# Performance work log

Hardware: AMD Instinct MI355X
Metric: run time of the kernel (lower is better)

The kernel has to match this reference:

```python
import jax, jax.numpy as jnp
import numpy as np

N_NODES = 50000
N_EDGES = 800000
IN_DIM = 128
HID = 32
HEADS = 4
OUT_DIM = 128
NEG_SLOPE = 0.2


def setup_inputs() -> dict:
    key = jax.random.key(0)
    ks = jax.random.split(key, 10)
    s = lambda fan_in: 1.0 / np.sqrt(fan_in)
    return {
        "x": jax.random.normal(ks[0], (N_NODES, IN_DIM), dtype=jnp.float32),
        "edge_index": jax.random.randint(ks[1], (2, N_EDGES), 0, N_NODES, dtype=jnp.int64),
        # encoder GATConv: in=IN_DIM, out=HID, heads=HEADS (concat)
        "W1": jax.random.normal(ks[2], (IN_DIM, HEADS * HID), dtype=jnp.float32) * s(IN_DIM),
        "att_src1": jax.random.normal(ks[3], (HEADS, HID), dtype=jnp.float32) * s(HID),
        "att_dst1": jax.random.normal(ks[4], (HEADS, HID), dtype=jnp.float32) * s(HID),
        "b1": jnp.zeros((HEADS * HID,), dtype=jnp.float32),
        # decoder GATConv: in=HEADS*HID, out=OUT_DIM, heads=1
        "W2": jax.random.normal(ks[5], (HEADS * HID, OUT_DIM), dtype=jnp.float32) * s(HEADS * HID),
        "att_src2": jax.random.normal(ks[6], (1, OUT_DIM), dtype=jnp.float32) * s(OUT_DIM),
        "att_dst2": jax.random.normal(ks[7], (1, OUT_DIM), dtype=jnp.float32) * s(OUT_DIM),
        "b2": jnp.zeros((OUT_DIM,), dtype=jnp.float32),
    }


def _gat_conv(x, src, dst, W, att_src, att_dst, bias, heads, out_ch):
    """PyG-style GATConv (v1), eval mode (dropout off), self-loops already in src/dst."""
    n = x.shape[0]
    h = (x @ W).reshape(n, heads, out_ch)                 # [N,H,C]
    a_src = jnp.einsum("nhc,hc->nh", h, att_src)          # [N,H]
    a_dst = jnp.einsum("nhc,hc->nh", h, att_dst)          # [N,H]
    e = jax.nn.leaky_relu(a_src[src] + a_dst[dst], NEG_SLOPE)  # [E,H]
    # segment softmax over destination neighborhoods
    e_max = jax.ops.segment_max(e, dst, num_segments=n)   # [N,H]
    e_exp = jnp.exp(e - e_max[dst])
    denom = jax.ops.segment_sum(e_exp, dst, num_segments=n)
    alpha = e_exp / (denom[dst] + 1e-16)                  # [E,H]
    msg = h[src] * alpha[:, :, None]                      # [E,H,C]
    out = jax.ops.segment_sum(msg, dst, num_segments=n)   # [N,H,C]
    return out.reshape(n, heads * out_ch) + bias


def reference(x, edge_index, W1, att_src1, att_dst1, b1, W2, att_src2, att_dst2, b2):
    n = x.shape[0]
    loops = jnp.arange(n, dtype=edge_index.dtype)
    src = jnp.concatenate([edge_index[0], loops])
    dst = jnp.concatenate([edge_index[1], loops])
    z = jax.nn.relu(_gat_conv(x, src, dst, W1, att_src1, att_dst1, b1, HEADS, HID))
    x_hat = jax.nn.relu(_gat_conv(z, src, dst, W2, att_src2, att_dst2, b2, 1, OUT_DIM))
    return x_hat
```

## Files before the change

kernel.cpp:

```cpp
#include <hip/hip_runtime.h>
#include <hip/hip_bf16.h>
#include <cstddef>

#define N_NODES 50000
#define N_EDGES_RAW 800000
#define E_TOT (N_EDGES_RAW + N_NODES)
#define DIM 128
#define NEG_SLOPE 0.2f

#define NBUCK 196
#define CHUNK 4096
#define NBLK_E ((E_TOT + CHUNK - 1) / CHUNK)
#define CONV_BLKS 3125
#define GB 782

typedef __attribute__((ext_vector_type(8))) short bf16x8;
typedef __attribute__((ext_vector_type(4))) float f32x4;

__device__ __forceinline__ ushort f2bf(float f) {
  unsigned u = __float_as_uint(f);
  return (ushort)((u + 0x7FFFu + ((u >> 16) & 1u)) >> 16);
}
__device__ __forceinline__ float bf2f_lo(uint u) {
  return __uint_as_float(u << 16);
}
__device__ __forceinline__ float bf2f_hi(uint u) {
  return __uint_as_float(u & 0xFFFF0000u);
}

__device__ __forceinline__ void get_edge(const int* __restrict__ ei, int is64,
                                         int e, int& s, int& d) {
  if (e >= N_EDGES_RAW) { s = e - N_EDGES_RAW; d = s; return; }
  if (is64) {
    s = ei[2 * (size_t)e];
    d = ei[2 * ((size_t)N_EDGES_RAW + (size_t)e)];
  } else {
    s = ei[e];
    d = ei[N_EDGES_RAW + e];
  }
}

__device__ __forceinline__ int detect_inline(const int* __restrict__ ei,
                                             int* sflag) {
  const int t = threadIdx.x;
  if (t < 64) {
    int hi = ei[2 * t + 1];
    unsigned long long b = __ballot(hi != 0);
    if (t == 0) *sflag = (b == 0ULL) ? 1 : 0;
  }
  __syncthreads();
  return *sflag;
}

__device__ __forceinline__ void prep_one(const float* __restrict__ w,
                                         const float* __restrict__ atts,
                                         const float* __restrict__ attd,
                                         ushort* __restrict__ wtx,
                                         int H, int idx) {
  const int c = idx >> 7, k = idx & 127;
  const int C = 128 / H;
  float v;
  if (c < 128) {
    v = w[k * 128 + c];
  } else if (c < 128 + H) {
    const int hd = c - 128;
    float s = 0.f;
    for (int j = 0; j < C; ++j) s += w[k * 128 + hd * C + j] * atts[hd * C + j];
    v = s;
  } else if (c < 128 + 2 * H) {
    const int hd = c - 128 - H;
    float s = 0.f;
    for (int j = 0; j < C; ++j) s += w[k * 128 + hd * C + j] * attd[hd * C + j];
    v = s;
  } else {
    v = 0.f;
  }
  wtx[idx] = f2bf(v);
}

__global__ __launch_bounds__(256) void mega_setup(
    const float* __restrict__ W1, const float* __restrict__ as1,
    const float* __restrict__ ad1, ushort* __restrict__ wtx1,
    const float* __restrict__ W2, const float* __restrict__ as2,
    const float* __restrict__ ad2, ushort* __restrict__ wtx2,
    const float* __restrict__ x, ushort* __restrict__ x_bf,
    const int* __restrict__ ei, int* __restrict__ hist_mat,
    unsigned* __restrict__ pairs) {
  const int b = blockIdx.x, t = threadIdx.x;
  if (b < 72) {
    prep_one(W1, as1, ad1, wtx1, 4, b * 256 + t);
  } else if (b < 144) {
    prep_one(W2, as2, ad2, wtx2, 1, (b - 72) * 256 + t);
  } else if (b < 144 + CONV_BLKS) {
    const int base = (b - 144) * 2048 + t * 8;
    float4 v0 = *(const float4*)(x + base);
    float4 v1 = *(const float4*)(x + base + 4);
    ushort u[8];
    u[0] = f2bf(v0.x); u[1] = f2bf(v0.y); u[2] = f2bf(v0.z); u[3] = f2bf(v0.w);
    u[4] = f2bf(v1.x); u[5] = f2bf(v1.y); u[6] = f2bf(v1.z); u[7] = f2bf(v1.w);
    *(uint4*)(x_bf + base) = *(const uint4*)u;
  } else {
    __shared__ int hist[NBUCK];
    __shared__ int sflag;
    const int cb = b - 144 - CONV_BLKS;
    if (t < NBUCK) hist[t] = 0;
    const int is64 = detect_inline(ei, &sflag);
    __syncthreads();
    const int e0 = cb * CHUNK;
#pragma unroll
    for (int i = 0; i < CHUNK / 256; ++i) {
      int e = e0 + i * 256 + t;
      if (e < E_TOT) {
        int s, d;
        get_edge(ei, is64, e, s, d);
        pairs[e] = (unsigned)s | ((unsigned)d << 16);
        atomicAdd(&hist[d >> 8], 1);
      }
    }
    __syncthreads();
    if (t < NBUCK) hist_mat[cb * NBUCK + t] = hist[t];
  }
}

__global__ __launch_bounds__(256) void bucket_scatter(
    const unsigned* __restrict__ pairs, const int* __restrict__ hist_mat,
    unsigned* __restrict__ tmp, int* __restrict__ bstart_g) {
  __shared__ int wtot[4];
  __shared__ int sbase[NBUCK];
  __shared__ int shist[NBUCK];
  const int b = blockIdx.x, t = threadIdx.x, lane = t & 63, wid = t >> 6;
  int tot = 0, pre = 0;
  if (t < NBUCK) {
    for (int bb = 0; bb < NBLK_E; ++bb) {
      int v = hist_mat[bb * NBUCK + t];
      pre += (bb < b) ? v : 0;
      tot += v;
    }
    shist[t] = 0;
  }
  int sc = tot;
#pragma unroll
  for (int m = 1; m < 64; m <<= 1) {
    int o = __shfl_up(sc, m, 64);
    if (lane >= m) sc += o;
  }
  if (lane == 63) wtot[wid] = sc;
  __syncthreads();
  int off = 0;
  for (int w = 0; w < wid; ++w) off += wtot[w];
  const int excl = off + sc - tot;
  if (t < NBUCK) sbase[t] = excl + pre;
  if (b == 0) {
    if (t < NBUCK) bstart_g[t] = excl;
    if (t == 255) bstart_g[NBUCK] = off + sc;
  }
  __syncthreads();
  const int e0 = b * CHUNK;
  unsigned pr_[CHUNK / 256];
  int rk[CHUNK / 256];
#pragma unroll
  for (int i = 0; i < CHUNK / 256; ++i) {
    int e = e0 + i * 256 + t;
    if (e < E_TOT) {
      unsigned pr = pairs[e];
      pr_[i] = pr;
      rk[i] = atomicAdd(&shist[pr >> 24], 1);
    }
  }
#pragma unroll
  for (int i = 0; i < CHUNK / 256; ++i) {
    int e = e0 + i * 256 + t;
    if (e < E_TOT) tmp[sbase[pr_[i] >> 24] + rk[i]] = pr_[i];
  }
}

__device__ __forceinline__ void bucket_sort_body(int b,
                                                 const unsigned* __restrict__ tmp,
                                                 const int* __restrict__ bstart,
                                                 unsigned* __restrict__ csr2,
                                                 int* __restrict__ rp,
                                                 int* __restrict__ deg) {
  __shared__ int cnt[256];
  __shared__ int cur[256];
  __shared__ int wtot2[4];
  const int t = threadIdx.x, lane = t & 63, wid = t >> 6;
  const int p0 = bstart[b], p1 = bstart[b + 1];
  cnt[t] = 0;
  __syncthreads();
  for (int j = p0 + t; j < p1; j += 256) {
    unsigned pr = tmp[j];
    atomicAdd(&cnt[(pr >> 16) & 255u], 1);
  }
  __syncthreads();
  int v = cnt[t];
  int sc = v;
#pragma unroll
  for (int m = 1; m < 64; m <<= 1) {
    int o = __shfl_up(sc, m, 64);
    if (lane >= m) sc += o;
  }
  if (lane == 63) wtot2[wid] = sc;
  __syncthreads();
  int off = 0;
  for (int w = 0; w < wid; ++w) off += wtot2[w];
  const int excl = off + sc - v;
  const int node = b * 256 + t;
  if (node < N_NODES) {
    deg[node] = v;
    rp[node] = p0 + excl;
  }
  cur[t] = excl;
  __syncthreads();
  for (int j = p0 + t; j < p1; j += 256) {
    unsigned pr = tmp[j];
    int ld = (int)((pr >> 16) & 255u);
    int r = atomicAdd(&cur[ld], 1);
    csr2[p0 + r] = pr;
  }
}

template <int H>
__device__ __forceinline__ void gemm_att_body(int blk,
                                              const ushort* __restrict__ in_bf,
                                              const ushort* __restrict__ wtx,
                                              ushort* __restrict__ h_bf,
                                              float* __restrict__ a_src,
                                              float* __restrict__ a_dst) {
  const int wid = threadIdx.x >> 6;
  const int lane = threadIdx.x & 63;
  const int tile = blk * 4 + wid;
  if (tile >= N_NODES / 16) return;
  const int row0 = tile * 16;
  const int rA = lane & 15;
  const int g = lane >> 4;

  f32x4 acc[9];
#pragma unroll
  for (int ct = 0; ct < 9; ++ct) acc[ct] = (f32x4){0.f, 0.f, 0.f, 0.f};

#pragma unroll
  for (int ks = 0; ks < 4; ++ks) {
    const int k0 = ks * 32 + g * 8;
    bf16x8 af = *(const bf16x8*)(in_bf + (size_t)(row0 + rA) * DIM + k0);
#pragma unroll
    for (int ct = 0; ct < 9; ++ct) {
      bf16x8 bf = *(const bf16x8*)(wtx + (size_t)(ct * 16 + rA) * 128 + k0);
      acc[ct] = __builtin_amdgcn_mfma_f32_16x16x32_bf16(af, bf, acc[ct], 0, 0, 0);
    }
  }

#pragma unroll
  for (int ct = 0; ct < 8; ++ct) {
#pragma unroll
    for (int r = 0; r < 4; ++r) {
      const int row = row0 + g * 4 + r;
      h_bf[(size_t)row * DIM + ct * 16 + rA] = f2bf(acc[ct][r]);
    }
  }
  if (rA < 2 * H) {
#pragma unroll
    for (int r = 0; r < 4; ++r) {
      const int row = row0 + g * 4 + r;
      if (rA < H)
        a_src[(size_t)row * H + rA] = acc[8][r];
      else
        a_dst[(size_t)row * H + (rA - H)] = acc[8][r];
    }
  }
}

__global__ __launch_bounds__(256) void gemm4_sort(
    const ushort* __restrict__ x_bf, const ushort* __restrict__ wtx1,
    ushort* __restrict__ h_bf, float* __restrict__ a_src,
    float* __restrict__ a_dst, const unsigned* __restrict__ tmp,
    const int* __restrict__ bstart, unsigned* __restrict__ csr2,
    int* __restrict__ rp, int* __restrict__ deg) {
  if (blockIdx.x < GB)
    gemm_att_body<4>(blockIdx.x, x_bf, wtx1, h_bf, a_src, a_dst);
  else
    bucket_sort_body(blockIdx.x - GB, tmp, bstart, csr2, rp, deg);
}

__global__ __launch_bounds__(256) void gemm_att1(const ushort* __restrict__ in_bf,
                                                 const ushort* __restrict__ wtx,
                                                 ushort* __restrict__ h_bf,
                                                 float* __restrict__ a_src,
                                                 float* __restrict__ a_dst) {
  gemm_att_body<1>(blockIdx.x, in_bf, wtx, h_bf, a_src, a_dst);
}

template <int H, bool OBF>
__global__ __launch_bounds__(256) void node_agg(const int* __restrict__ rp,
                                                const int* __restrict__ deg,
                                                const unsigned* __restrict__ csr2,
                                                const ushort* __restrict__ h_bf,
                                                const float* __restrict__ a_src,
                                                const float* __restrict__ a_dst,
                                                const float* __restrict__ bias,
                                                void* __restrict__ outp) {
  __shared__ float p_lds[4][H][68];
  __shared__ int s_lds[4][64];
  const int wid = threadIdx.x >> 6;
  const int lane = threadIdx.x & 63;
  const int node = blockIdx.x * 4 + wid;
  if (node >= N_NODES) return;
  const int head = (H == 4) ? (lane >> 4) : 0;
  const int beg = rp[node];
  const int dg = deg[node];

  float ad[H];
#pragma unroll
  for (int h = 0; h < H; ++h) ad[h] = a_dst[(size_t)node * H + h];

  float sden = 0.f, ax = 0.f, ay = 0.f;

  for (int c0 = 0; c0 < dg; c0 += 64) {
    const int cnt = min(64, dg - c0);
    if (lane < cnt) {
      int s = (int)(csr2[beg + c0 + lane] & 0xFFFFu);
      s_lds[wid][lane] = s;
      if (H == 4) {
        float4 as4 = ((const float4*)a_src)[s];
        float vv[4] = {as4.x, as4.y, as4.z, as4.w};
#pragma unroll
        for (int h = 0; h < 4; ++h) {
          float v = vv[h] + ad[h];
          v = v > 0.f ? v : NEG_SLOPE * v;
          v = fminf(fmaxf(v, -60.f), 80.f);
          p_lds[wid][h][lane] = __expf(v);
        }
      } else {
        float v = a_src[s] + ad[0];
        v = v > 0.f ? v : NEG_SLOPE * v;
        v = fminf(fmaxf(v, -60.f), 80.f);
        p_lds[wid][0][lane] = __expf(v);
      }
    }
    int j = 0;
    for (; j + 8 <= cnt; j += 8) {
#pragma unroll
      for (int u = 0; u < 8; ++u) {
        int s = s_lds[wid][j + u];
        float p = p_lds[wid][head][j + u];
        uint hv = *(const uint*)(h_bf + (size_t)s * DIM + 2 * lane);
        ax += p * bf2f_lo(hv);
        ay += p * bf2f_hi(hv);
        sden += p;
      }
    }
    for (; j < cnt; ++j) {
      int s = s_lds[wid][j];
      float p = p_lds[wid][head][j];
      uint hv = *(const uint*)(h_bf + (size_t)s * DIM + 2 * lane);
      ax += p * bf2f_lo(hv);
      ay += p * bf2f_hi(hv);
      sden += p;
    }
  }

  const float inv = 1.f / sden;
  float2 bv = ((const float2*)bias)[lane];
  float ox = fmaxf(ax * inv + bv.x, 0.f);
  float oy = fmaxf(ay * inv + bv.y, 0.f);
  if (OBF) {
    uint u = (uint)f2bf(ox) | ((uint)f2bf(oy) << 16);
    ((uint*)((ushort*)outp + (size_t)node * DIM))[lane] = u;
  } else {
    ((float2*)((float*)outp + (size_t)node * DIM))[lane] = make_float2(ox, oy);
  }
}

extern "C" void kernel_launch(void* const* d_in, const int* in_sizes, int n_in,
                              void* d_out, int out_size, void* d_ws, size_t ws_size,
                              hipStream_t stream) {
  const float* x   = (const float*)d_in[0];
  const int*   ei  = (const int*)d_in[1];
  const float* W1  = (const float*)d_in[2];
  const float* as1 = (const float*)d_in[3];
  const float* ad1 = (const float*)d_in[4];
  const float* b1  = (const float*)d_in[5];
  const float* W2  = (const float*)d_in[6];
  const float* as2 = (const float*)d_in[7];
  const float* ad2 = (const float*)d_in[8];
  const float* b2  = (const float*)d_in[9];
  float* out = (float*)d_out;

  char* ws = (char*)d_ws;
  const size_t F_H = (size_t)N_NODES * DIM;
  ushort*   h_bf    = (ushort*)ws;
  ushort*   z_bf    = h_bf + F_H;
  ushort*   x_bf    = z_bf + F_H;
  float*    a_src   = (float*)(x_bf + F_H);
  float*    a_dst   = a_src + 200000;
  int*      deg     = (int*)(a_dst + 200000);
  int*      rp      = deg + N_NODES;
  unsigned* csr2    = (unsigned*)(rp + N_NODES);
  unsigned* tmp     = csr2 + E_TOT;
  unsigned* pairs   = tmp + E_TOT;
  int*      hist_mat= (int*)(pairs + E_TOT);
  int*      bstart  = hist_mat + NBLK_E * NBUCK;
  ushort*   wtx1    = (ushort*)(bstart + NBUCK + 3);
  ushort*   wtx2    = wtx1 + 144 * 128;

  const int MEGA = 144 + CONV_BLKS + NBLK_E;
  const int AGG_B = (N_NODES + 3) / 4;

  hipLaunchKernelGGL(mega_setup, dim3(MEGA), dim3(256), 0, stream,
                     W1, as1, ad1, wtx1, W2, as2, ad2, wtx2, x, x_bf, ei,
                     hist_mat, pairs);
  hipLaunchKernelGGL(bucket_scatter, dim3(NBLK_E), dim3(256), 0, stream,
                     pairs, hist_mat, tmp, bstart);
  hipLaunchKernelGGL(gemm4_sort, dim3(GB + NBUCK), dim3(256), 0, stream,
                     x_bf, wtx1, h_bf, a_src, a_dst, tmp, bstart, csr2, rp, deg);
  hipLaunchKernelGGL((node_agg<4, true>), dim3(AGG_B), dim3(256), 0, stream,
                     rp, deg, csr2, h_bf, a_src, a_dst, b1, z_bf);

  hipLaunchKernelGGL(gemm_att1, dim3(GB), dim3(256), 0, stream,
                     z_bf, wtx2, h_bf, a_src, a_dst);
  hipLaunchKernelGGL((node_agg<1, false>), dim3(AGG_B), dim3(256), 0, stream,
                     rp, deg, csr2, h_bf, a_src, a_dst, b2, out);
}
```

Baseline: 164.1 us.

## Reorder decoder layer to aggregate first, then apply W2 in the aggregation epilogue

```diff
diff --git a/kernel.cpp b/kernel.cpp
--- a/kernel.cpp
+++ b/kernel.cpp
@@ -79,20 +79,35 @@
 }
 
 __global__ __launch_bounds__(256) void mega_setup(
+    const int* __restrict__ ei, int* __restrict__ hist_mat,
+    unsigned* __restrict__ pairs,
     const float* __restrict__ W1, const float* __restrict__ as1,
-    const float* __restrict__ ad1, ushort* __restrict__ wtx1,
+    const float* __restrict__ ad1,
     const float* __restrict__ W2, const float* __restrict__ as2,
-    const float* __restrict__ ad2, ushort* __restrict__ wtx2,
+    const float* __restrict__ ad2,
     const float* __restrict__ x, ushort* __restrict__ x_bf,
-    const int* __restrict__ ei, int* __restrict__ hist_mat,
-    unsigned* __restrict__ pairs) {
+    ushort* __restrict__ wtx1, ushort* __restrict__ wtx2,
+    float* __restrict__ w_as2, float* __restrict__ w_ad2) {
   const int b = blockIdx.x, t = threadIdx.x;
   if (b < 72) {
     prep_one(W1, as1, ad1, wtx1, 4, b * 256 + t);
-  } else if (b < 144) {
-    prep_one(W2, as2, ad2, wtx2, 1, (b - 72) * 256 + t);
-  } else if (b < 144 + CONV_BLKS) {
-    const int base = (b - 144) * 2048 + t * 8;
+  } else if (b < 136) {
+    const int idx = (b - 72) * 256 + t;
+    const int c = idx >> 7, k = idx & 127;
+    wtx2[idx] = f2bf(W2[k * 128 + c]);
+  } else if (b == 136) {
+    if (t < 128) {
+      float s2 = 0.f, d2 = 0.f;
+      for (int c = 0; c < 128; ++c) {
+        float w = W2[t * 128 + c];
+        s2 += w * as2[c];
+        d2 += w * ad2[c];
+      }
+      w_as2[t] = s2;
+      w_ad2[t] = d2;
+    }
+  } else if (b < 137 + CONV_BLKS) {
+    const int base = (b - 137) * 2048 + t * 8;
     float4 v0 = *(const float4*)(x + base);
     float4 v1 = *(const float4*)(x + base + 4);
     ushort u[8];
@@ -102,7 +117,7 @@
   } else {
     __shared__ int hist[NBUCK];
     __shared__ int sflag;
-    const int cb = b - 144 - CONV_BLKS;
+    const int cb = b - 137 - CONV_BLKS;
     if (t < NBUCK) hist[t] = 0;
     const int is64 = detect_inline(ei, &sflag);
     __syncthreads();
@@ -219,13 +234,12 @@
   }
 }
 
-template <int H>
-__device__ __forceinline__ void gemm_att_body(int blk,
-                                              const ushort* __restrict__ in_bf,
-                                              const ushort* __restrict__ wtx,
-                                              ushort* __restrict__ h_bf,
-                                              float* __restrict__ a_src,
-                                              float* __restrict__ a_dst) {
+__device__ __forceinline__ void gemm_att_body4(int blk,
+                                               const ushort* __restrict__ in_bf,
+                                               const ushort* __restrict__ wtx,
+                                               ushort* __restrict__ h_bf,
+                                               float* __restrict__ a_src,
+                                               float* __restrict__ a_dst) {
   const int wid = threadIdx.x >> 6;
   const int lane = threadIdx.x & 63;
   const int tile = blk * 4 + wid;
@@ -257,14 +271,14 @@
       h_bf[(size_t)row * DIM + ct * 16 + rA] = f2bf(acc[ct][r]);
     }
   }
-  if (rA < 2 * H) {
+  if (rA < 8) {
 #pragma unroll
     for (int r = 0; r < 4; ++r) {
       const int row = row0 + g * 4 + r;
-      if (rA < H)
-        a_src[(size_t)row * H + rA] = acc[8][r];
+      if (rA < 4)
+        a_src[(size_t)row * 4 + rA] = acc[8][r];
       else
-        a_dst[(size_t)row * H + (rA - H)] = acc[8][r];
+        a_dst[(size_t)row * 4 + (rA - 4)] = acc[8][r];
     }
   }
 }
@@ -276,41 +290,30 @@
     const int* __restrict__ bstart, unsigned* __restrict__ csr2,
     int* __restrict__ rp, int* __restrict__ deg) {
   if (blockIdx.x < GB)
-    gemm_att_body<4>(blockIdx.x, x_bf, wtx1, h_bf, a_src, a_dst);
+    gemm_att_body4(blockIdx.x, x_bf, wtx1, h_bf, a_src, a_dst);
   else
     bucket_sort_body(blockIdx.x - GB, tmp, bstart, csr2, rp, deg);
 }
 
-__global__ __launch_bounds__(256) void gemm_att1(const ushort* __restrict__ in_bf,
-                                                 const ushort* __restrict__ wtx,
-                                                 ushort* __restrict__ h_bf,
-                                                 float* __restrict__ a_src,
-                                                 float* __restrict__ a_dst) {
-  gemm_att_body<1>(blockIdx.x, in_bf, wtx, h_bf, a_src, a_dst);
-}
-
-template <int H, bool OBF>
-__global__ __launch_bounds__(256) void node_agg(const int* __restrict__ rp,
-                                                const int* __restrict__ deg,
-                                                const unsigned* __restrict__ csr2,
-                                                const ushort* __restrict__ h_bf,
-                                                const float* __restrict__ a_src,
-                                                const float* __restrict__ a_dst,
-                                                const float* __restrict__ bias,
-                                                void* __restrict__ outp) {
-  __shared__ float p_lds[4][H][68];
+__global__ __launch_bounds__(256) void node_agg_l1(
+    const int* __restrict__ rp, const int* __restrict__ deg,
+    const unsigned* __restrict__ csr2, const ushort* __restrict__ h_bf,
+    const float* __restrict__ a_srcv, const float* __restrict__ a_dstv,
+    const float* __restrict__ bias, const float* __restrict__ w_as2,
+    const float* __restrict__ w_ad2, ushort* __restrict__ z_bf,
+    float* __restrict__ a_src2, float* __restrict__ a_dst2) {
+  __shared__ float p_lds[4][4][68];
   __shared__ int s_lds[4][64];
   const int wid = threadIdx.x >> 6;
   const int lane = threadIdx.x & 63;
   const int node = blockIdx.x * 4 + wid;
-  if (node >= N_NODES) return;
-  const int head = (H == 4) ? (lane >> 4) : 0;
+  const int head = lane >> 4;
   const int beg = rp[node];
   const int dg = deg[node];
 
-  float ad[H];
-#pragma unroll
-  for (int h = 0; h < H; ++h) ad[h] = a_dst[(size_t)node * H + h];
+  float ad[4];
+#pragma unroll
+  for (int h = 0; h < 4; ++h) ad[h] = a_dstv[(size_t)node * 4 + h];
 
   float sden = 0.f, ax = 0.f, ay = 0.f;
 
@@ -319,21 +322,14 @@
     if (lane < cnt) {
       int s = (int)(csr2[beg + c0 + lane] & 0xFFFFu);
       s_lds[wid][lane] = s;
-      if (H == 4) {
-        float4 as4 = ((const float4*)a_src)[s];
-        float vv[4] = {as4.x, as4.y, as4.z, as4.w};
-#pragma unroll
-        for (int h = 0; h < 4; ++h) {
-          float v = vv[h] + ad[h];
-          v = v > 0.f ? v : NEG_SLOPE * v;
-          v = fminf(fmaxf(v, -60.f), 80.f);
-          p_lds[wid][h][lane] = __expf(v);
-        }
-      } else {
-        float v = a_src[s] + ad[0];
+      float4 as4 = ((const float4*)a_srcv)[s];
+      float vv[4] = {as4.x, as4.y, as4.z, as4.w};
+#pragma unroll
+      for (int h = 0; h < 4; ++h) {
+        float v = vv[h] + ad[h];
         v = v > 0.f ? v : NEG_SLOPE * v;
         v = fminf(fmaxf(v, -60.f), 80.f);
-        p_lds[wid][0][lane] = __expf(v);
+        p_lds[wid][h][lane] = __expf(v);
       }
     }
     int j = 0;
@@ -362,11 +358,102 @@
   float2 bv = ((const float2*)bias)[lane];
   float ox = fmaxf(ax * inv + bv.x, 0.f);
   float oy = fmaxf(ay * inv + bv.y, 0.f);
-  if (OBF) {
-    uint u = (uint)f2bf(ox) | ((uint)f2bf(oy) << 16);
-    ((uint*)((ushort*)outp + (size_t)node * DIM))[lane] = u;
-  } else {
-    ((float2*)((float*)outp + (size_t)node * DIM))[lane] = make_float2(ox, oy);
+  uint u = (uint)f2bf(ox) | ((uint)f2bf(oy) << 16);
+  ((uint*)(z_bf + (size_t)node * DIM))[lane] = u;
+
+  float2 ws = ((const float2*)w_as2)[lane];
+  float2 wd = ((const float2*)w_ad2)[lane];
+  float ps = ox * ws.x + oy * ws.y;
+  float pd = ox * wd.x + oy * wd.y;
+#pragma unroll
+  for (int m = 1; m < 64; m <<= 1) {
+    ps += __shfl_xor(ps, m);
+    pd += __shfl_xor(pd, m);
+  }
+  if (lane == 0) {
+    a_src2[node] = ps;
+    a_dst2[node] = pd;
+  }
+}
+
+__global__ __launch_bounds__(256) void node_agg_l2(
+    const int* __restrict__ rp, const int* __restrict__ deg,
+    const unsigned* __restrict__ csr2, const ushort* __restrict__ z_bf,
+    const float* __restrict__ a_src2, const float* __restrict__ a_dst2,
+    const ushort* __restrict__ wtx2, const float* __restrict__ bias,
+    float* __restrict__ outp) {
+  __shared__ float p_lds[4][68];
+  __shared__ int s_lds[4][64];
+  __shared__ ushort u_lds[16][136];
+  const int wid = threadIdx.x >> 6;
+  const int lane = threadIdx.x & 63;
+  const int node = blockIdx.x * 4 + wid;
+  const int beg = rp[node];
+  const int dg = deg[node];
+  const float ad = a_dst2[node];
+
+  float sden = 0.f, ax = 0.f, ay = 0.f;
+
+  for (int c0 = 0; c0 < dg; c0 += 64) {
+    const int cnt = min(64, dg - c0);
+    if (lane < cnt) {
+      int s = (int)(csr2[beg + c0 + lane] & 0xFFFFu);
+      s_lds[wid][lane] = s;
+      float v = a_src2[s] + ad;
+      v = v > 0.f ? v : NEG_SLOPE * v;
+      v = fminf(fmaxf(v, -60.f), 80.f);
+      p_lds[wid][lane] = __expf(v);
+    }
+    int j = 0;
+    for (; j + 8 <= cnt; j += 8) {
+#pragma unroll
+      for (int u = 0; u < 8; ++u) {
+        int s = s_lds[wid][j + u];
+        float p = p_lds[wid][j + u];
+        uint hv = *(const uint*)(z_bf + (size_t)s * DIM + 2 * lane);
+        ax += p * bf2f_lo(hv);
+        ay += p * bf2f_hi(hv);
+        sden += p;
+      }
+    }
+    for (; j < cnt; ++j) {
+      int s = s_lds[wid][j];
+      float p = p_lds[wid][j];
+      uint hv = *(const uint*)(z_bf + (size_t)s * DIM + 2 * lane);
+      ax += p * bf2f_lo(hv);
+      ay += p * bf2f_hi(hv);
+      sden += p;
+    }
+  }
+
+  const float inv = 1.f / sden;
+  uint upk = (uint)f2bf(ax * inv) | ((uint)f2bf(ay * inv) << 16);
+  ((uint*)(&u_lds[wid][0]))[lane] = upk;
+  __syncthreads();
+
+  const int rA = lane & 15;
+  const int g = lane >> 4;
+  f32x4 acc0 = {0.f, 0.f, 0.f, 0.f}, acc1 = acc0;
+#pragma unroll
+  for (int ks = 0; ks < 4; ++ks) {
+    const int k0 = ks * 32 + g * 8;
+    bf16x8 af = *(const bf16x8*)&u_lds[rA][k0];
+    bf16x8 b0 = *(const bf16x8*)(wtx2 + (size_t)(wid * 32 + rA) * 128 + k0);
+    bf16x8 b1 = *(const bf16x8*)(wtx2 + (size_t)(wid * 32 + 16 + rA) * 128 + k0);
+    acc0 = __builtin_amdgcn_mfma_f32_16x16x32_bf16(af, b0, acc0, 0, 0, 0);
+    acc1 = __builtin_amdgcn_mfma_f32_16x16x32_bf16(af, b1, acc1, 0, 0, 0);
+  }
+  if (g == 0) {
+#pragma unroll
+    for (int q = 0; q < 2; ++q) {
+      const int col = wid * 32 + q * 16 + rA;
+      const float bv = bias[col];
+      const f32x4 a = q == 0 ? acc0 : acc1;
+#pragma unroll
+      for (int r = 0; r < 4; ++r) {
+        outp[(size_t)(blockIdx.x * 4 + r) * DIM + col] = fmaxf(a[r] + bv, 0.f);
+      }
+    }
   }
 }
 
@@ -390,9 +477,11 @@
   ushort*   h_bf    = (ushort*)ws;
   ushort*   z_bf    = h_bf + F_H;
   ushort*   x_bf    = z_bf + F_H;
-  float*    a_src   = (float*)(x_bf + F_H);
-  float*    a_dst   = a_src + 200000;
-  int*      deg     = (int*)(a_dst + 200000);
+  float*    a_src1  = (float*)(x_bf + F_H);
+  float*    a_dst1  = a_src1 + 200000;
+  float*    a_src2  = a_dst1 + 200000;
+  float*    a_dst2  = a_src2 + N_NODES;
+  int*      deg     = (int*)(a_dst2 + N_NODES);
   int*      rp      = deg + N_NODES;
   unsigned* csr2    = (unsigned*)(rp + N_NODES);
   unsigned* tmp     = csr2 + E_TOT;
@@ -401,22 +490,22 @@
   int*      bstart  = hist_mat + NBLK_E * NBUCK;
   ushort*   wtx1    = (ushort*)(bstart + NBUCK + 3);
   ushort*   wtx2    = wtx1 + 144 * 128;
-
-  const int MEGA = 144 + CONV_BLKS + NBLK_E;
-  const int AGG_B = (N_NODES + 3) / 4;
+  float*    w_as2   = (float*)(wtx2 + 128 * 128);
+  float*    w_ad2   = w_as2 + 128;
+
+  const int MEGA = 137 + CONV_BLKS + NBLK_E;
+  const int AGG_B = N_NODES / 4;
 
   hipLaunchKernelGGL(mega_setup, dim3(MEGA), dim3(256), 0, stream,
-                     W1, as1, ad1, wtx1, W2, as2, ad2, wtx2, x, x_bf, ei,
-                     hist_mat, pairs);
+                     ei, hist_mat, pairs, W1, as1, ad1, W2, as2, ad2,
+                     x, x_bf, wtx1, wtx2, w_as2, w_ad2);
   hipLaunchKernelGGL(bucket_scatter, dim3(NBLK_E), dim3(256), 0, stream,
                      pairs, hist_mat, tmp, bstart);
   hipLaunchKernelGGL(gemm4_sort, dim3(GB + NBUCK), dim3(256), 0, stream,
-                     x_bf, wtx1, h_bf, a_src, a_dst, tmp, bstart, csr2, rp, deg);
-  hipLaunchKernelGGL((node_agg<4, true>), dim3(AGG_B), dim3(256), 0, stream,
-                     rp, deg, csr2, h_bf, a_src, a_dst, b1, z_bf);
-
-  hipLaunchKernelGGL(gemm_att1, dim3(GB), dim3(256), 0, stream,
-                     z_bf, wtx2, h_bf, a_src, a_dst);
-  hipLaunchKernelGGL((node_agg<1, false>), dim3(AGG_B), dim3(256), 0, stream,
-                     rp, deg, csr2, h_bf, a_src, a_dst, b2, out);
-}
+                     x_bf, wtx1, h_bf, a_src1, a_dst1, tmp, bstart, csr2, rp, deg);
+  hipLaunchKernelGGL(node_agg_l1, dim3(AGG_B), dim3(256), 0, stream,
+                     rp, deg, csr2, h_bf, a_src1, a_dst1, b1, w_as2, w_ad2,
+                     z_bf, a_src2, a_dst2);
+  hipLaunchKernelGGL(node_agg_l2, dim3(AGG_B), dim3(256), 0, stream,
+                     rp, deg, csr2, z_bf, a_src2, a_dst2, wtx2, b2, out);
+}
```

Result: slower. 176.9 us (+7.8%).
